# Kernel tuning notes

Hardware: AMD Instinct MI355X
Metric: run time of the kernel (lower is better)

## Reference

```python
import jax, jax.numpy as jnp
import numpy as np

N_T = 100000   # transaction nodes
N_A = 50000    # account nodes
F = 256        # raw feature dim
H = 256        # hidden_dim
E = 800000     # edges per edge type


def setup_inputs() -> dict:
    key = jax.random.key(0)
    ks = jax.random.split(key, 14)
    s = 1.0 / np.sqrt(F)
    return {
        "x_tx": jax.random.normal(ks[0], (N_T, F), jnp.float32),
        "x_acc": jax.random.normal(ks[1], (N_A, F), jnp.float32),
        "edge_at_src": jax.random.randint(ks[2], (E,), 0, N_A, jnp.int32),
        "edge_at_dst": jax.random.randint(ks[3], (E,), 0, N_T, jnp.int32),
        "edge_ta_src": jax.random.randint(ks[4], (E,), 0, N_T, jnp.int32),
        "edge_ta_dst": jax.random.randint(ks[5], (E,), 0, N_A, jnp.int32),
        "W_l_at": jax.random.normal(ks[6], (F, H), jnp.float32) * s,
        "b_l_at": jnp.zeros((H,), jnp.float32),
        "W_r_at": jax.random.normal(ks[7], (F, H), jnp.float32) * s,
        "W_l_ta": jax.random.normal(ks[8], (F, H), jnp.float32) * s,
        "b_l_ta": jnp.zeros((H,), jnp.float32),
        "W_r_ta": jax.random.normal(ks[9], (F, H), jnp.float32) * s,
        "W_out": jax.random.normal(ks[10], (H, 1), jnp.float32) * (1.0 / np.sqrt(H)),
        "b_out": jnp.zeros((1,), jnp.float32),
    }


def _sage(x_src, x_dst, src_idx, dst_idx, W_l, b_l, W_r, num_dst):
    # PyG SAGEConv (mean aggr): lin_l(mean_j x_src[j]) + lin_r(x_dst)
    msgs = x_src[src_idx]  # [E, F] gather
    summed = jax.ops.segment_sum(msgs, dst_idx, num_segments=num_dst)  # [num_dst, F]
    cnt = jax.ops.segment_sum(jnp.ones((src_idx.shape[0],), x_src.dtype), dst_idx,
                              num_segments=num_dst)
    mean = summed / jnp.maximum(cnt, 1.0)[:, None]  # isolated dst -> zeros
    return mean @ W_l + b_l + x_dst @ W_r


def reference(x_tx, x_acc, edge_at_src, edge_at_dst, edge_ta_src, edge_ta_dst,
              W_l_at, b_l_at, W_r_at, W_l_ta, b_l_ta, W_r_ta, W_out, b_out):
    # account -> transaction SAGEConv
    h_tx = _sage(x_acc, x_tx, edge_at_src, edge_at_dst, W_l_at, b_l_at, W_r_at, N_T)
    # transaction -> account SAGEConv (computed as in HeteroConv, though unused downstream)
    h_acc = _sage(x_tx, x_acc, edge_ta_src, edge_ta_dst, W_l_ta, b_l_ta, W_r_ta, N_A)
    tx_x = jax.nn.relu(h_tx)
    _ = jax.nn.relu(h_acc)
    logits = (tx_x @ W_out + b_out)[:, 0]  # squeeze(-1)
    return logits, tx_x
```

## Files before the change

### kernel.cpp

```cpp
#include <hip/hip_runtime.h>
#include <hip/hip_bf16.h>

typedef __bf16 bf16x8_t __attribute__((ext_vector_type(8)));
typedef __bf16 bf16x4_t __attribute__((ext_vector_type(4)));
typedef float f32x4_t __attribute__((ext_vector_type(4)));

#define M_TX 100000
#define N_AC 50000
#define FDIM 256
#define HDIM 256
#define KTOT 512
#define SCAN_NBLK ((M_TX + 1023) / 1024)

__global__ __launch_bounds__(256) void initk2(float* __restrict__ logits,
                                              int* __restrict__ hist,
                                              int* __restrict__ fill,
                                              const float* __restrict__ b_out) {
    int i = blockIdx.x * 256 + threadIdx.x;
    if (i < M_TX) {
        logits[i] = b_out[0];
        hist[i] = 0;
        fill[i] = 0;
    }
}

__global__ __launch_bounds__(256) void transw(const float* __restrict__ Wl,
                                              const float* __restrict__ Wr,
                                              __bf16* __restrict__ WT) {
    int t = blockIdx.x * 256 + threadIdx.x;
    if (t >= FDIM * HDIM) return;
    int k = t >> 8;
    int n = t & 255;
    WT[n * KTOT + k]        = (__bf16)Wl[k * HDIM + n];
    WT[n * KTOT + 256 + k]  = (__bf16)Wr[k * HDIM + n];
}

__global__ __launch_bounds__(256) void histk(const int* __restrict__ edst,
                                             int* __restrict__ hist, int E) {
    int e = blockIdx.x * 256 + threadIdx.x;
    if (e >= E) return;
    atomicAdd(&hist[edst[e]], 1);
}

__global__ __launch_bounds__(1024) void scan1k(const int* __restrict__ hist,
                                               int* __restrict__ row_start,
                                               int* __restrict__ partials) {
    __shared__ int tmp[1024];
    const int b = blockIdx.x;
    const int t = threadIdx.x;
    const int i = b * 1024 + t;
    int v = (i < M_TX) ? hist[i] : 0;
    tmp[t] = v;
    __syncthreads();
    for (int off = 1; off < 1024; off <<= 1) {
        int u = (t >= off) ? tmp[t - off] : 0;
        __syncthreads();
        tmp[t] += u;
        __syncthreads();
    }
    if (i < M_TX) row_start[i] = tmp[t] - v;
    if (t == 1023) partials[b] = tmp[1023];
}

__global__ __launch_bounds__(128) void scan2k(int* __restrict__ partials,
                                              int* __restrict__ row_start) {
    __shared__ int tmp[128];
    const int t = threadIdx.x;
    int v = (t < SCAN_NBLK) ? partials[t] : 0;
    tmp[t] = v;
    __syncthreads();
    for (int off = 1; off < 128; off <<= 1) {
        int u = (t >= off) ? tmp[t - off] : 0;
        __syncthreads();
        tmp[t] += u;
        __syncthreads();
    }
    if (t < SCAN_NBLK) partials[t] = tmp[t] - v;
    if (t == 127) row_start[M_TX] = tmp[127];
}

__global__ __launch_bounds__(1024) void scan3k(int* __restrict__ row_start,
                                               const int* __restrict__ partials) {
    const int i = blockIdx.x * 1024 + threadIdx.x;
    if (i < M_TX) row_start[i] += partials[blockIdx.x];
}

__global__ __launch_bounds__(256) void scatterk(const int* __restrict__ esrc,
                                                const int* __restrict__ edst,
                                                const int* __restrict__ row_start,
                                                int* __restrict__ fill,
                                                int* __restrict__ sorted_src, int E) {
    int e = blockIdx.x * 256 + threadIdx.x;
    if (e >= E) return;
    int d = edst[e];
    int pos = row_start[d] + atomicAdd(&fill[d], 1);
    sorted_src[pos] = esrc[e];
}

__global__ __launch_bounds__(256) void gatherk(const float* __restrict__ x_acc,
                                               const int* __restrict__ sorted_src,
                                               const int* __restrict__ row_start,
                                               float* __restrict__ summed) {
    int gw = (blockIdx.x * 256 + threadIdx.x) >> 6;
    if (gw >= M_TX) return;
    int lane = threadIdx.x & 63;
    int start = row_start[gw];
    int end = row_start[gw + 1];
    f32x4_t acc = {0.f, 0.f, 0.f, 0.f};
    for (int base = start; base < end; base += 64) {
        int n = end - base; if (n > 64) n = 64;
        int s = 0;
        if (base + lane < end) s = sorted_src[base + lane];
        for (int j = 0; j < n; ++j) {
            int sj = __shfl(s, j);
            const f32x4_t v = *(const f32x4_t*)(x_acc + (long)sj * FDIM + lane * 4);
            acc.x += v.x; acc.y += v.y; acc.z += v.z; acc.w += v.w;
        }
    }
    *(f32x4_t*)(summed + (long)gw * FDIM + lane * 4) = acc;
}

__global__ __launch_bounds__(512) void gemmk(const float* __restrict__ x_tx,
                                             const float* __restrict__ summed,
                                             const int* __restrict__ row_start,
                                             const __bf16* __restrict__ WT,
                                             const float* __restrict__ b_l,
                                             const float* __restrict__ W_out,
                                             float* __restrict__ tx_out,
                                             float* __restrict__ logits) {
    __shared__ __bf16 As[128][72];
    __shared__ __bf16 Bs[256][72];

    const int m0 = blockIdx.x * 128;
    const int tid = threadIdx.x;
    const int wid = tid >> 6;
    const int lane = tid & 63;
    const int wm = wid >> 2;
    const int wn = wid & 3;
    const int lc = lane & 15;
    const int lr = lane >> 4;

    f32x4_t acc[4][4];
#pragma unroll
    for (int i = 0; i < 4; ++i)
#pragma unroll
        for (int j = 0; j < 4; ++j) acc[i][j] = (f32x4_t){0.f, 0.f, 0.f, 0.f};

    const int ar = tid >> 2;
    const int acq = tid & 3;
    const int arm = m0 + ar;
    const bool arow_ok = arm < M_TX;
    float invc;
    {
        int idx = arow_ok ? arm : (M_TX - 1);
        int c = row_start[idx + 1] - row_start[idx];
        invc = 1.0f / fmaxf((float)c, 1.0f);
    }

    for (int kc = 0; kc < 8; ++kc) {
        __syncthreads();
        {
            const bool first = kc < 4;
            const int kb = (kc & 3) * 64;
            const float sc = first ? invc : 1.0f;
            const float* base = first ? (summed + (long)arm * FDIM + kb)
                                      : (x_tx + (long)arm * FDIM + kb);
#pragma unroll
            for (int c4 = 0; c4 < 4; ++c4) {
                int kk = acq * 16 + c4 * 4;
                f32x4_t v = {0.f, 0.f, 0.f, 0.f};
                if (arow_ok) v = *(const f32x4_t*)(base + kk);
                bf16x4_t w;
                w[0] = (__bf16)(v.x * sc);
                w[1] = (__bf16)(v.y * sc);
                w[2] = (__bf16)(v.z * sc);
                w[3] = (__bf16)(v.w * sc);
                *(bf16x4_t*)(&As[ar][kk]) = w;
            }
        }
#pragma unroll
        for (int i = 0; i < 4; ++i) {
            int t2 = tid + i * 512;
            int n = t2 >> 3;
            int c = t2 & 7;
            bf16x8_t v = *(const bf16x8_t*)(WT + n * KTOT + kc * 64 + c * 8);
            *(bf16x8_t*)(&Bs[n][c * 8]) = v;
        }
        __syncthreads();
        const int kfr = lr * 8;
#pragma unroll
        for (int kk = 0; kk < 2; ++kk) {
            bf16x8_t af[4], bfr[4];
#pragma unroll
            for (int f = 0; f < 4; ++f) {
                af[f] = *(const bf16x8_t*)(&As[wm * 64 + f * 16 + lc][kk * 32 + kfr]);
                bfr[f] = *(const bf16x8_t*)(&Bs[wn * 64 + f * 16 + lc][kk * 32 + kfr]);
            }
#pragma unroll
            for (int fm = 0; fm < 4; ++fm)
#pragma unroll
                for (int fn = 0; fn < 4; ++fn)
                    acc[fm][fn] = __builtin_amdgcn_mfma_f32_16x16x32_bf16(
                        af[fm], bfr[fn], acc[fm][fn], 0, 0, 0);
        }
    }

    float wout[4], bl[4];
#pragma unroll
    for (int fn = 0; fn < 4; ++fn) {
        int col = wn * 64 + fn * 16 + lc;
        wout[fn] = W_out[col];
        bl[fn] = b_l[col];
    }
#pragma unroll
    for (int fm = 0; fm < 4; ++fm) {
        float part[4] = {0.f, 0.f, 0.f, 0.f};
#pragma unroll
        for (int fn = 0; fn < 4; ++fn) {
            int col = wn * 64 + fn * 16 + lc;
#pragma unroll
            for (int r = 0; r < 4; ++r) {
                int row = m0 + wm * 64 + fm * 16 + lr * 4 + r;
                float h = acc[fm][fn][r] + bl[fn];
                h = fmaxf(h, 0.0f);
                if (row < M_TX) tx_out[(long)row * HDIM + col] = h;
                part[r] += h * wout[fn];
            }
        }
#pragma unroll
        for (int r = 0; r < 4; ++r) {
            float p = part[r];
            p += __shfl_xor(p, 1);
            p += __shfl_xor(p, 2);
            p += __shfl_xor(p, 4);
            p += __shfl_xor(p, 8);
            int row = m0 + wm * 64 + fm * 16 + lr * 4 + r;
            if (lc == 0 && row < M_TX) unsafeAtomicAdd(logits + row, p);
        }
    }
}

extern "C" void kernel_launch(void* const* d_in, const int* in_sizes, int n_in,
                              void* d_out, int out_size, void* d_ws, size_t ws_size,
                              hipStream_t stream) {
    const float* x_tx  = (const float*)d_in[0];
    const float* x_acc = (const float*)d_in[1];
    const int* e_src   = (const int*)d_in[2];
    const int* e_dst   = (const int*)d_in[3];
    const float* W_l   = (const float*)d_in[6];
    const float* b_l   = (const float*)d_in[7];
    const float* W_r   = (const float*)d_in[8];
    const float* W_out = (const float*)d_in[12];
    const float* b_out = (const float*)d_in[13];

    float* out = (float*)d_out;
    float* logits = out;
    float* summed = out + M_TX;

    char* ws = (char*)d_ws;
    __bf16* WT       = (__bf16*)ws;
    int* row_start   = (int*)(ws + 256 * 1024);
    int* fill        = (int*)(ws + 256 * 1024 + 400 * 1024 + 1024);
    int* sorted_src  = (int*)(ws + 256 * 1024 + 800 * 1024 + 2048);
    int* histp       = (int*)(ws + 256 * 1024 + 800 * 1024 + 2048 + 3200 * 1024 + 1024);
    int* partials    = (int*)(ws + 256 * 1024 + 800 * 1024 + 2048 + 3200 * 1024 + 1024
                              + 400 * 1024 + 1024);

    const int E = in_sizes[2];

    hipLaunchKernelGGL(initk2, dim3((M_TX + 255) / 256), dim3(256), 0, stream,
                       logits, histp, fill, b_out);
    hipLaunchKernelGGL(transw, dim3((FDIM * HDIM + 255) / 256), dim3(256), 0, stream,
                       W_l, W_r, WT);
    hipLaunchKernelGGL(histk, dim3((E + 255) / 256), dim3(256), 0, stream,
                       e_dst, histp, E);
    hipLaunchKernelGGL(scan1k, dim3(SCAN_NBLK), dim3(1024), 0, stream,
                       histp, row_start, partials);
    hipLaunchKernelGGL(scan2k, dim3(1), dim3(128), 0, stream, partials, row_start);
    hipLaunchKernelGGL(scan3k, dim3(SCAN_NBLK), dim3(1024), 0, stream,
                       row_start, partials);
    hipLaunchKernelGGL(scatterk, dim3((E + 255) / 256), dim3(256), 0, stream,
                       e_src, e_dst, row_start, fill, sorted_src, E);
    hipLaunchKernelGGL(gatherk, dim3(M_TX / 4), dim3(256), 0, stream,
                       x_acc, sorted_src, row_start, summed);
    hipLaunchKernelGGL(gemmk, dim3((M_TX + 127) / 128), dim3(512), 0, stream,
                       x_tx, summed, row_start, WT, b_l, W_out, out + M_TX, logits);
}
```

Before: 478.3 us.

## Pre-convert features to bf16 and store bf16 mean for gather and GEMM

Adds a conversion kernel that casts x_acc (and x_tx if workspace allows) to bf16 in workspace, so the edge gather reads half the bytes per neighbour row. The gather now applies the mean division and writes a bf16 mean buffer, and the GEMM loads bf16 A tiles directly instead of converting fp32 on the fly. Each stage is gated on workspace size, with the old fp32 paths kept as fallbacks. Conversions add extra full passes over x_acc and x_tx, and summing bf16-rounded inputs slightly changes numerics.

```diff
diff --git a/kernel.cpp b/kernel.cpp
--- a/kernel.cpp
+++ b/kernel.cpp
@@ -11,6 +11,13 @@
 #define HDIM 256
 #define KTOT 512
 #define SCAN_NBLK ((M_TX + 1023) / 1024)
+
+__device__ inline bf16x8_t bzero8() {
+    bf16x8_t v;
+#pragma unroll
+    for (int z = 0; z < 8; ++z) v[z] = (__bf16)0.f;
+    return v;
+}
 
 __global__ __launch_bounds__(256) void initk2(float* __restrict__ logits,
                                               int* __restrict__ hist,
@@ -33,6 +40,18 @@
     int n = t & 255;
     WT[n * KTOT + k]        = (__bf16)Wl[k * HDIM + n];
     WT[n * KTOT + 256 + k]  = (__bf16)Wr[k * HDIM + n];
+}
+
+__global__ __launch_bounds__(256) void cvtk(const float* __restrict__ src,
+                                            __bf16* __restrict__ dst, int n4) {
+    int stride = gridDim.x * 256;
+    for (int i = blockIdx.x * 256 + threadIdx.x; i < n4; i += stride) {
+        f32x4_t v = ((const f32x4_t*)src)[i];
+        bf16x4_t w;
+        w[0] = (__bf16)v.x; w[1] = (__bf16)v.y;
+        w[2] = (__bf16)v.z; w[3] = (__bf16)v.w;
+        ((bf16x4_t*)dst)[i] = w;
+    }
 }
 
 __global__ __launch_bounds__(256) void histk(const int* __restrict__ edst,
@@ -98,30 +117,56 @@
 }
 
 __global__ __launch_bounds__(256) void gatherk(const float* __restrict__ x_acc,
+                                               const __bf16* __restrict__ xab,
                                                const int* __restrict__ sorted_src,
                                                const int* __restrict__ row_start,
-                                               float* __restrict__ summed) {
+                                               float* __restrict__ summed,
+                                               __bf16* __restrict__ meanb) {
     int gw = (blockIdx.x * 256 + threadIdx.x) >> 6;
     if (gw >= M_TX) return;
     int lane = threadIdx.x & 63;
     int start = row_start[gw];
     int end = row_start[gw + 1];
     f32x4_t acc = {0.f, 0.f, 0.f, 0.f};
-    for (int base = start; base < end; base += 64) {
-        int n = end - base; if (n > 64) n = 64;
-        int s = 0;
-        if (base + lane < end) s = sorted_src[base + lane];
-        for (int j = 0; j < n; ++j) {
-            int sj = __shfl(s, j);
-            const f32x4_t v = *(const f32x4_t*)(x_acc + (long)sj * FDIM + lane * 4);
-            acc.x += v.x; acc.y += v.y; acc.z += v.z; acc.w += v.w;
-        }
-    }
-    *(f32x4_t*)(summed + (long)gw * FDIM + lane * 4) = acc;
+    if (xab) {
+        for (int base = start; base < end; base += 64) {
+            int n = end - base; if (n > 64) n = 64;
+            int s = 0;
+            if (base + lane < end) s = sorted_src[base + lane];
+            for (int j = 0; j < n; ++j) {
+                int sj = __shfl(s, j);
+                const bf16x4_t v = *(const bf16x4_t*)(xab + (long)sj * FDIM + lane * 4);
+                acc.x += (float)v[0]; acc.y += (float)v[1];
+                acc.z += (float)v[2]; acc.w += (float)v[3];
+            }
+        }
+    } else {
+        for (int base = start; base < end; base += 64) {
+            int n = end - base; if (n > 64) n = 64;
+            int s = 0;
+            if (base + lane < end) s = sorted_src[base + lane];
+            for (int j = 0; j < n; ++j) {
+                int sj = __shfl(s, j);
+                const f32x4_t v = *(const f32x4_t*)(x_acc + (long)sj * FDIM + lane * 4);
+                acc.x += v.x; acc.y += v.y; acc.z += v.z; acc.w += v.w;
+            }
+        }
+    }
+    if (meanb) {
+        float inv = 1.0f / fmaxf((float)(end - start), 1.0f);
+        bf16x4_t w;
+        w[0] = (__bf16)(acc.x * inv); w[1] = (__bf16)(acc.y * inv);
+        w[2] = (__bf16)(acc.z * inv); w[3] = (__bf16)(acc.w * inv);
+        *(bf16x4_t*)(meanb + (long)gw * FDIM + lane * 4) = w;
+    } else {
+        *(f32x4_t*)(summed + (long)gw * FDIM + lane * 4) = acc;
+    }
 }
 
 __global__ __launch_bounds__(512) void gemmk(const float* __restrict__ x_tx,
+                                             const __bf16* __restrict__ xtb,
                                              const float* __restrict__ summed,
+                                             const __bf16* __restrict__ meanb,
                                              const int* __restrict__ row_start,
                                              const __bf16* __restrict__ WT,
                                              const float* __restrict__ b_l,
@@ -150,8 +195,8 @@
     const int acq = tid & 3;
     const int arm = m0 + ar;
     const bool arow_ok = arm < M_TX;
-    float invc;
-    {
+    float invc = 1.0f;
+    if (!meanb) {
         int idx = arow_ok ? arm : (M_TX - 1);
         int c = row_start[idx + 1] - row_start[idx];
         invc = 1.0f / fmaxf((float)c, 1.0f);
@@ -162,20 +207,32 @@
         {
             const bool first = kc < 4;
             const int kb = (kc & 3) * 64;
-            const float sc = first ? invc : 1.0f;
-            const float* base = first ? (summed + (long)arm * FDIM + kb)
-                                      : (x_tx + (long)arm * FDIM + kb);
-#pragma unroll
-            for (int c4 = 0; c4 < 4; ++c4) {
-                int kk = acq * 16 + c4 * 4;
-                f32x4_t v = {0.f, 0.f, 0.f, 0.f};
-                if (arow_ok) v = *(const f32x4_t*)(base + kk);
-                bf16x4_t w;
-                w[0] = (__bf16)(v.x * sc);
-                w[1] = (__bf16)(v.y * sc);
-                w[2] = (__bf16)(v.z * sc);
-                w[3] = (__bf16)(v.w * sc);
-                *(bf16x4_t*)(&As[ar][kk]) = w;
+            const __bf16* bsrc = first ? meanb : xtb;
+            if (bsrc) {
+                const __bf16* bb = bsrc + (long)arm * FDIM + kb + acq * 16;
+                bf16x8_t v0 = bzero8(), v1 = bzero8();
+                if (arow_ok) {
+                    v0 = *(const bf16x8_t*)bb;
+                    v1 = *(const bf16x8_t*)(bb + 8);
+                }
+                *(bf16x8_t*)(&As[ar][acq * 16]) = v0;
+                *(bf16x8_t*)(&As[ar][acq * 16 + 8]) = v1;
+            } else {
+                const float sc = first ? invc : 1.0f;
+                const float* base = first ? (summed + (long)arm * FDIM + kb)
+                                          : (x_tx + (long)arm * FDIM + kb);
+#pragma unroll
+                for (int c4 = 0; c4 < 4; ++c4) {
+                    int kk = acq * 16 + c4 * 4;
+                    f32x4_t v = {0.f, 0.f, 0.f, 0.f};
+                    if (arow_ok) v = *(const f32x4_t*)(base + kk);
+                    bf16x4_t w;
+                    w[0] = (__bf16)(v.x * sc);
+                    w[1] = (__bf16)(v.y * sc);
+                    w[2] = (__bf16)(v.z * sc);
+                    w[3] = (__bf16)(v.w * sc);
+                    *(bf16x4_t*)(&As[ar][kk]) = w;
+                }
             }
         }
 #pragma unroll
@@ -258,13 +315,40 @@
     float* summed = out + M_TX;
 
     char* ws = (char*)d_ws;
-    __bf16* WT       = (__bf16*)ws;
-    int* row_start   = (int*)(ws + 256 * 1024);
-    int* fill        = (int*)(ws + 256 * 1024 + 400 * 1024 + 1024);
-    int* sorted_src  = (int*)(ws + 256 * 1024 + 800 * 1024 + 2048);
-    int* histp       = (int*)(ws + 256 * 1024 + 800 * 1024 + 2048 + 3200 * 1024 + 1024);
-    int* partials    = (int*)(ws + 256 * 1024 + 800 * 1024 + 2048 + 3200 * 1024 + 1024
-                              + 400 * 1024 + 1024);
+    size_t off = 0;
+    auto alloc = [&](size_t bytes) {
+        size_t o = off;
+        off = (off + bytes + 255) & ~(size_t)255;
+        return o;
+    };
+    size_t o_WT       = alloc((size_t)HDIM * KTOT * 2);
+    size_t o_rowstart = alloc(((size_t)M_TX + 1) * 4);
+    size_t o_fill     = alloc((size_t)M_TX * 4);
+    size_t o_sorted   = alloc((size_t)800000 * 4);
+    size_t o_hist     = alloc((size_t)M_TX * 4);
+    size_t o_part     = alloc((size_t)SCAN_NBLK * 4);
+    size_t base_end   = off;
+    size_t o_xa       = alloc((size_t)N_AC * FDIM * 2);
+    size_t lvlA_end   = off;
+    size_t o_mean     = alloc((size_t)M_TX * FDIM * 2);
+    size_t lvlB_end   = off;
+    size_t o_xt       = alloc((size_t)M_TX * FDIM * 2);
+    size_t lvlC_end   = off;
+    (void)base_end;
+
+    __bf16* WT       = (__bf16*)(ws + o_WT);
+    int* row_start   = (int*)(ws + o_rowstart);
+    int* fill        = (int*)(ws + o_fill);
+    int* sorted_src  = (int*)(ws + o_sorted);
+    int* histp       = (int*)(ws + o_hist);
+    int* partials    = (int*)(ws + o_part);
+
+    const bool lvlA = ws_size >= lvlA_end;
+    const bool lvlB = ws_size >= lvlB_end;
+    const bool lvlC = ws_size >= lvlC_end;
+    __bf16* xab   = lvlA ? (__bf16*)(ws + o_xa)   : nullptr;
+    __bf16* meanb = lvlB ? (__bf16*)(ws + o_mean) : nullptr;
+    __bf16* xtb   = lvlC ? (__bf16*)(ws + o_xt)   : nullptr;
 
     const int E = in_sizes[2];
 
@@ -272,6 +356,12 @@
                        logits, histp, fill, b_out);
     hipLaunchKernelGGL(transw, dim3((FDIM * HDIM + 255) / 256), dim3(256), 0, stream,
                        W_l, W_r, WT);
+    if (xab)
+        hipLaunchKernelGGL(cvtk, dim3(2048), dim3(256), 0, stream,
+                           x_acc, xab, N_AC * FDIM / 4);
+    if (xtb)
+        hipLaunchKernelGGL(cvtk, dim3(2048), dim3(256), 0, stream,
+                           x_tx, xtb, M_TX * FDIM / 4);
     hipLaunchKernelGGL(histk, dim3((E + 255) / 256), dim3(256), 0, stream,
                        e_dst, histp, E);
     hipLaunchKernelGGL(scan1k, dim3(SCAN_NBLK), dim3(1024), 0, stream,
@@ -282,7 +372,8 @@
     hipLaunchKernelGGL(scatterk, dim3((E + 255) / 256), dim3(256), 0, stream,
                        e_src, e_dst, row_start, fill, sorted_src, E);
     hipLaunchKernelGGL(gatherk, dim3(M_TX / 4), dim3(256), 0, stream,
-                       x_acc, sorted_src, row_start, summed);
+                       x_acc, xab, sorted_src, row_start, summed, meanb);
     hipLaunchKernelGGL(gemmk, dim3((M_TX + 127) / 128), dim3(512), 0, stream,
-                       x_tx, summed, row_start, WT, b_l, W_out, out + M_TX, logits);
-}
+                       x_tx, xtb, summed, meanb, row_start, WT, b_l, W_out,
+                       out + M_TX, logits);
+}
```

Result: faster. 462.8 us (-3.2%).
